# Performance work log

Measured on AMD Instinct MI355X. Metric: run time of the kernel, lower is better.

## Reference

```python
import jax, jax.numpy as jnp
import numpy as np

N_NODES = 50000
N_EDGES = 600000
D = 128
NEG_SLOPE = 0.2


def _gat_conv(x, src, dst, W, a_src, a_dst, b):
    # x: [N, D]; src/dst: [E'] (self-loops included); PyG GATConv, heads=1
    h = x @ W                               # [N, D]
    alpha_s = h @ a_src                     # [N]
    alpha_d = h @ a_dst                     # [N]
    e = alpha_s[src] + alpha_d[dst]         # [E'] raw scores per edge j->i
    e = jnp.where(e > 0, e, NEG_SLOPE * e)  # LeakyReLU(0.2)
    # segment softmax over incoming edges of each dst node
    m = jax.ops.segment_max(e, dst, num_segments=N_NODES)
    ex = jnp.exp(e - m[dst])
    denom = jax.ops.segment_sum(ex, dst, num_segments=N_NODES)
    alpha = ex / denom[dst]                 # [E']
    out = jax.ops.segment_sum(alpha[:, None] * h[src], dst, num_segments=N_NODES)
    return out + b


def setup_inputs() -> dict:
    key = jax.random.key(0)
    ks = jax.random.split(key, 10)
    scale = 1.0 / np.sqrt(D)
    x = jax.random.normal(ks[0], (N_NODES, D), dtype=jnp.float32)
    edge_index = jax.random.randint(ks[1], (2, N_EDGES), 0, N_NODES, dtype=jnp.int64)
    params = {}
    for i, base in ((1, 2), (2, 6)):
        params[f"W{i}"] = jax.random.normal(ks[base], (D, D), dtype=jnp.float32) * scale
        params[f"a_src{i}"] = jax.random.normal(ks[base + 1], (D,), dtype=jnp.float32) * scale
        params[f"a_dst{i}"] = jax.random.normal(ks[base + 2], (D,), dtype=jnp.float32) * scale
        params[f"b{i}"] = jnp.zeros((D,), dtype=jnp.float32)
    return {"x": x, "edge_index": edge_index, **params}


def reference(x, edge_index, W1, a_src1, a_dst1, b1, W2, a_src2, a_dst2, b2):
    # add self-loops (PyG GATConv default add_self_loops=True)
    loops = jnp.arange(N_NODES, dtype=edge_index.dtype)
    src = jnp.concatenate([edge_index[0], loops])
    dst = jnp.concatenate([edge_index[1], loops])
    h = _gat_conv(x, src, dst, W1, a_src1, a_dst1, b1)
    h = jax.nn.relu(h)  # BasicGNN act between layers, none after last
    out = _gat_conv(h, src, dst, W2, a_src2, a_dst2, b2)
    return out
```

## Files before the change

kernel.cpp:

```cpp
#include <hip/hip_runtime.h>
#include <hip/hip_bf16.h>

#define D 128
#define NEG_SLOPE 0.2f
#define AGG_CHUNK 128
#define CHUNKB 4096
#define CAPN 64

typedef short bf16x8 __attribute__((ext_vector_type(8)));
typedef unsigned short ushort8 __attribute__((ext_vector_type(8)));
typedef float f32x4 __attribute__((ext_vector_type(4)));

__device__ inline unsigned short bfbits(float f) {
  __hip_bfloat16 b = __float2bfloat16(f);
  return *(unsigned short*)&b;
}

__device__ inline float2 bf2_to_f2(unsigned v) {
  return make_float2(__uint_as_float(v << 16), __uint_as_float(v & 0xffff0000u));
}


template <bool RELU, bool BF16IN>
__device__ __forceinline__ void gemm_body(ushort* Wt, int tile,
                                          const void* __restrict__ in,
                                          const float* __restrict__ W,
                                          const float* __restrict__ a_s,
                                          const float* __restrict__ a_d,
                                          ushort* __restrict__ hb,
                                          float* __restrict__ as_out,
                                          float* __restrict__ ad_out, int N) {
  int tid = threadIdx.x;
  for (int u = tid; u < 2048; u += 256) {
    int kp = u >> 5, cg = u & 31;
    int k = kp * 2;
    float4 w0 = *(const float4*)(W + (size_t)k * D + cg * 4);
    float4 w1 = *(const float4*)(W + (size_t)(k + 1) * D + cg * 4);
    float v0[4] = {w0.x, w0.y, w0.z, w0.w};
    float v1[4] = {w1.x, w1.y, w1.z, w1.w};
    #pragma unroll
    for (int i = 0; i < 4; ++i) {
      int c = cg * 4 + i;
      unsigned word = (unsigned)bfbits(v0[i]) | ((unsigned)bfbits(v1[i]) << 16);
      int byte = c * 256 + ((k * 2) ^ ((c & 7) << 4));
      *(unsigned*)((char*)Wt + byte) = word;
    }
  }
  __syncthreads();

  int wave = tid >> 6, lane = tid & 63;
  int lrow = lane & 15, lgrp = lane >> 4;
  int r0 = tile * 128 + wave * 32;
  int rowA[2];
  rowA[0] = min(r0 + lrow, N - 1);
  rowA[1] = min(r0 + 16 + lrow, N - 1);

  f32x4 acc[2][8];
  #pragma unroll
  for (int t = 0; t < 2; ++t)
    #pragma unroll
    for (int nt = 0; nt < 8; ++nt) acc[t][nt] = (f32x4){0.f, 0.f, 0.f, 0.f};

  #pragma unroll
  for (int ks = 0; ks < 4; ++ks) {
    bf16x8 af[2];
    #pragma unroll
    for (int t = 0; t < 2; ++t) {
      if (BF16IN) {
        const ushort* arow = (const ushort*)in + (size_t)rowA[t] * D;
        ushort8 u = *(const ushort8*)(arow + ks * 32 + lgrp * 8);
        if (RELU) {
          #pragma unroll
          for (int j = 0; j < 8; ++j) u[j] = (u[j] & 0x8000u) ? 0 : u[j];
        }
        #pragma unroll
        for (int j = 0; j < 8; ++j) af[t][j] = (short)u[j];
      } else {
        const float* arow = (const float*)in + (size_t)rowA[t] * D;
        float4 a0 = *(const float4*)(arow + ks * 32 + lgrp * 8);
        float4 a1 = *(const float4*)(arow + ks * 32 + lgrp * 8 + 4);
        if (RELU) {
          a0.x = fmaxf(a0.x, 0.f); a0.y = fmaxf(a0.y, 0.f);
          a0.z = fmaxf(a0.z, 0.f); a0.w = fmaxf(a0.w, 0.f);
          a1.x = fmaxf(a1.x, 0.f); a1.y = fmaxf(a1.y, 0.f);
          a1.z = fmaxf(a1.z, 0.f); a1.w = fmaxf(a1.w, 0.f);
        }
        af[t][0] = (short)bfbits(a0.x); af[t][1] = (short)bfbits(a0.y);
        af[t][2] = (short)bfbits(a0.z); af[t][3] = (short)bfbits(a0.w);
        af[t][4] = (short)bfbits(a1.x); af[t][5] = (short)bfbits(a1.y);
        af[t][6] = (short)bfbits(a1.z); af[t][7] = (short)bfbits(a1.w);
      }
    }
    #pragma unroll
    for (int nt = 0; nt < 8; ++nt) {
      int c = nt * 16 + lrow;
      int kb = (ks * 64 + lgrp * 16) ^ ((c & 7) << 4);
      bf16x8 bfr = *(const bf16x8*)((const char*)Wt + c * 256 + kb);
      acc[0][nt] = __builtin_amdgcn_mfma_f32_16x16x32_bf16(af[0], bfr, acc[0][nt], 0, 0, 0);
      acc[1][nt] = __builtin_amdgcn_mfma_f32_16x16x32_bf16(af[1], bfr, acc[1][nt], 0, 0, 0);
    }
  }

  float ps[2][4] = {{0.f,0.f,0.f,0.f},{0.f,0.f,0.f,0.f}};
  float pd[2][4] = {{0.f,0.f,0.f,0.f},{0.f,0.f,0.f,0.f}};
  #pragma unroll
  for (int nt = 0; nt < 8; ++nt) {
    float asc = a_s[nt * 16 + lrow];
    float adc = a_d[nt * 16 + lrow];
    #pragma unroll
    for (int t = 0; t < 2; ++t) {
      #pragma unroll
      for (int r = 0; r < 4; ++r) {
        float v = acc[t][nt][r];
        ps[t][r] += v * asc;
        pd[t][r] += v * adc;
        int row = r0 + t * 16 + lgrp * 4 + r;
        if (row < N) hb[(size_t)row * D + nt * 16 + lrow] = bfbits(v);
      }
    }
  }
  #pragma unroll
  for (int mk = 1; mk < 16; mk <<= 1) {
    #pragma unroll
    for (int t = 0; t < 2; ++t)
      #pragma unroll
      for (int r = 0; r < 4; ++r) {
        ps[t][r] += __shfl_xor(ps[t][r], mk);
        pd[t][r] += __shfl_xor(pd[t][r], mk);
      }
  }
  if (lrow == 0) {
    #pragma unroll
    for (int t = 0; t < 2; ++t)
      #pragma unroll
      for (int r = 0; r < 4; ++r) {
        int row = r0 + t * 16 + lgrp * 4 + r;
        if (row < N) { as_out[row] = ps[t][r]; ad_out[row] = pd[t][r]; }
      }
  }
}


__global__ __launch_bounds__(256) void scatter_gemm_kernel(const int* __restrict__ ei,
                                                           int* __restrict__ cursor,
                                                           ushort* __restrict__ stage16,
                                                           int E, int total, int nblk,
                                                           const float* __restrict__ in,
                                                           const float* __restrict__ W,
                                                           const float* __restrict__ a_s,
                                                           const float* __restrict__ a_d,
                                                           ushort* __restrict__ hb,
                                                           float* __restrict__ as_out,
                                                           float* __restrict__ ad_out, int N) {
  if ((int)blockIdx.x < nblk) {
    int base = blockIdx.x * CHUNKB;
    int end = min(base + CHUNKB, total);
    for (int e = base + threadIdx.x; e < end; e += 256) {
      int src, dst;
      if (e < E) { src = ei[e]; dst = ei[E + e]; }
      else       { src = dst = e - E; }
      int pos = atomicAdd(&cursor[dst], 1);
      if (pos < CAPN) stage16[(size_t)dst * CAPN + pos] = (ushort)src;
    }
  } else {
    __shared__ ushort Wt[D * D];
    gemm_body<false, false>(Wt, blockIdx.x - nblk, in, W, a_s, a_d, hb, as_out, ad_out, N);
  }
}


__global__ __launch_bounds__(256) void gemm_bf16_kernel(const ushort* __restrict__ in,
                                                        const float* __restrict__ W,
                                                        const float* __restrict__ a_s,
                                                        const float* __restrict__ a_d,
                                                        ushort* __restrict__ hb,
                                                        float* __restrict__ as_out,
                                                        float* __restrict__ ad_out, int N) {
  __shared__ ushort Wt[D * D];
  gemm_body<true, true>(Wt, blockIdx.x, in, W, a_s, a_d, hb, as_out, ad_out, N);
}


template <typename TOUT>
__global__ __launch_bounds__(256) void agg_kernel(const ushort* __restrict__ hb,
                                                  const int* __restrict__ cursor,
                                                  const ushort* __restrict__ stage16,
                                                  const float* __restrict__ as_,
                                                  const float* __restrict__ ad_,
                                                  const float* __restrict__ bias,
                                                  TOUT* __restrict__ out, int N) {
  int wid = threadIdx.x >> 6;
  int lane = threadIdx.x & 63;
  int n = blockIdx.x * 4 + wid;
  if (n >= N) return;
  int deg = cursor[n];
  if (deg > CAPN) deg = CAPN;
  int start = n * CAPN;
  float adv = ad_[n];
  int g = lane >> 4;
  int fl = lane & 15;

  float accf[8] = {0.f, 0.f, 0.f, 0.f, 0.f, 0.f, 0.f, 0.f};
  float denom;

  if (deg <= 32) {
    int s0 = 0;
    float asv = 0.f;
    if (lane < deg) {
      s0 = (int)stage16[start + lane];
      asv = as_[s0];
    }
    uint4 pv[8];
    #pragma unroll
    for (int it = 0; it < 8; ++it) {
      int idx = it * 4 + g;
      int sv = __shfl(s0, idx < 64 ? idx : 0);
      if (idx < deg)
        pv[it] = *(const uint4*)(hb + (size_t)sv * D + fl * 8);
    }
    float w0 = 0.f;
    if (lane < deg) {
      float sc = asv + adv;
      sc = sc > 0.f ? sc : NEG_SLOPE * sc;
      w0 = __expf(sc);
    }
    denom = w0;
    #pragma unroll
    for (int off = 32; off; off >>= 1) denom += __shfl_xor(denom, off);
    #pragma unroll
    for (int it = 0; it < 8; ++it) {
      int idx = it * 4 + g;
      float wv = __shfl(w0, idx < 64 ? idx : 0);
      if (idx < deg) {
        float2 f0 = bf2_to_f2(pv[it].x), f1 = bf2_to_f2(pv[it].y);
        float2 f2 = bf2_to_f2(pv[it].z), f3 = bf2_to_f2(pv[it].w);
        accf[0] += wv * f0.x; accf[1] += wv * f0.y;
        accf[2] += wv * f1.x; accf[3] += wv * f1.y;
        accf[4] += wv * f2.x; accf[5] += wv * f2.y;
        accf[6] += wv * f3.x; accf[7] += wv * f3.y;
      }
    }
  } else {
    int end = start + deg;
    int e0 = start + lane;
    int s0 = 0;
    float w0 = 0.f;
    if (e0 < end) {
      s0 = (int)stage16[e0];
      float sc = as_[s0] + adv;
      sc = sc > 0.f ? sc : NEG_SLOPE * sc;
      w0 = __expf(sc);
    }
    denom = w0;
    #pragma unroll
    for (int off = 32; off; off >>= 1) denom += __shfl_xor(denom, off);
    for (int i = 0; i < deg; i += 4) {
      int idx = i + g;
      int   sv = __shfl(s0, idx < 64 ? idx : 0);
      float wv = __shfl(w0, idx < 64 ? idx : 0);
      if (idx < deg) {
        uint4 hv = *(const uint4*)(hb + (size_t)sv * D + fl * 8);
        float2 f0 = bf2_to_f2(hv.x), f1 = bf2_to_f2(hv.y);
        float2 f2 = bf2_to_f2(hv.z), f3 = bf2_to_f2(hv.w);
        accf[0] += wv * f0.x; accf[1] += wv * f0.y;
        accf[2] += wv * f1.x; accf[3] += wv * f1.y;
        accf[4] += wv * f2.x; accf[5] += wv * f2.y;
        accf[6] += wv * f3.x; accf[7] += wv * f3.y;
      }
    }
  }

  #pragma unroll
  for (int j = 0; j < 8; ++j) accf[j] += __shfl_xor(accf[j], 16);
  #pragma unroll
  for (int j = 0; j < 8; ++j) accf[j] += __shfl_xor(accf[j], 32);

  if (g == 0) {
    float inv = 1.f / denom;
    float4 b0 = *(const float4*)(bias + fl * 8);
    float4 b1 = *(const float4*)(bias + fl * 8 + 4);
    float o[8] = {accf[0] * inv + b0.x, accf[1] * inv + b0.y,
                  accf[2] * inv + b0.z, accf[3] * inv + b0.w,
                  accf[4] * inv + b1.x, accf[5] * inv + b1.y,
                  accf[6] * inv + b1.z, accf[7] * inv + b1.w};
    if (sizeof(TOUT) == 4) {
      float* op = (float*)out + (size_t)n * D + fl * 8;
      *(float4*)op = make_float4(o[0], o[1], o[2], o[3]);
      *(float4*)(op + 4) = make_float4(o[4], o[5], o[6], o[7]);
    } else {
      ushort8 u;
      #pragma unroll
      for (int j = 0; j < 8; ++j) u[j] = bfbits(o[j]);
      *(ushort8*)((ushort*)out + (size_t)n * D + fl * 8) = u;
    }
  }
}


extern "C" void kernel_launch(void* const* d_in, const int* in_sizes, int n_in,
                              void* d_out, int out_size, void* d_ws, size_t ws_size,
                              hipStream_t stream) {
  const float* x   = (const float*)d_in[0];
  const int*   ei  = (const int*)d_in[1];
  const float* W1  = (const float*)d_in[2];
  const float* as1 = (const float*)d_in[3];
  const float* ad1 = (const float*)d_in[4];
  const float* b1  = (const float*)d_in[5];
  const float* W2  = (const float*)d_in[6];
  const float* as2 = (const float*)d_in[7];
  const float* ad2 = (const float*)d_in[8];
  const float* b2  = (const float*)d_in[9];

  int N = in_sizes[0] / D;
  int E = in_sizes[1] / 2;
  int total = E + N;
  int nblk = (total + CHUNKB - 1) / CHUNKB;
  int nbG = (N + 127) / 128;

  char* ws = (char*)d_ws;
  size_t off = 0;
  auto alloc = [&](size_t bytes) {
    void* p = ws + off;
    off = (off + bytes + 255) & ~(size_t)255;
    return p;
  };
  ushort*   hb      = (ushort*)alloc((size_t)N * D * sizeof(ushort));
  ushort*   tmpb    = (ushort*)alloc((size_t)N * D * sizeof(ushort));
  float*    alpha_s = (float*)alloc((size_t)N * sizeof(float));
  float*    alpha_d = (float*)alloc((size_t)N * sizeof(float));
  int*      cursor  = (int*)alloc((size_t)N * sizeof(int));
  ushort*   stage16 = (ushort*)alloc((size_t)N * CAPN * sizeof(ushort));

  hipMemsetAsync(cursor, 0, (size_t)N * sizeof(int), stream);
  scatter_gemm_kernel<<<nblk + nbG, 256, 0, stream>>>(ei, cursor, stage16, E, total, nblk,
                                                      x, W1, as1, ad1, hb, alpha_s, alpha_d, N);

  agg_kernel<ushort><<<(N + 3) / 4, 256, 0, stream>>>(hb, cursor, stage16, alpha_s, alpha_d,
                                                      b1, tmpb, N);

  gemm_bf16_kernel<<<nbG, 256, 0, stream>>>(tmpb, W2, as2, ad2, hb, alpha_s, alpha_d, N);

  agg_kernel<float><<<(N + 3) / 4, 256, 0, stream>>>(hb, cursor, stage16, alpha_s, alpha_d,
                                                     b2, (float*)d_out, N);
}
```

Measured before the change: 109.5 us.

## Split fused scatter/GEMM kernel, batch scatter atomics, vectorize weight staging

Splits the combined scatter-plus-GEMM launch into a separate edge scatter kernel and a GEMM kernel. The scatter now gives each block 1024 edges and each thread four edges, issuing all loads, then all atomics, then all stores, so more memory operations are in flight. The weight transpose into shared memory now packs eight k values per thread and does one 16-byte LDS store instead of four 4-byte stores. The split adds a kernel launch and removes the overlap the fused launch had between scatter and GEMM blocks.

```diff
diff --git a/kernel.cpp b/kernel.cpp
--- a/kernel.cpp
+++ b/kernel.cpp
@@ -3,8 +3,7 @@
 
 #define D 128
 #define NEG_SLOPE 0.2f
-#define AGG_CHUNK 128
-#define CHUNKB 4096
+#define CHUNKS 1024
 #define CAPN 64
 
 typedef short bf16x8 __attribute__((ext_vector_type(8)));
@@ -32,19 +31,22 @@
                                           float* __restrict__ ad_out, int N) {
   int tid = threadIdx.x;
   for (int u = tid; u < 2048; u += 256) {
-    int kp = u >> 5, cg = u & 31;
-    int k = kp * 2;
-    float4 w0 = *(const float4*)(W + (size_t)k * D + cg * 4);
-    float4 w1 = *(const float4*)(W + (size_t)(k + 1) * D + cg * 4);
-    float v0[4] = {w0.x, w0.y, w0.z, w0.w};
-    float v1[4] = {w1.x, w1.y, w1.z, w1.w};
-    #pragma unroll
-    for (int i = 0; i < 4; ++i) {
-      int c = cg * 4 + i;
-      unsigned word = (unsigned)bfbits(v0[i]) | ((unsigned)bfbits(v1[i]) << 16);
-      int byte = c * 256 + ((k * 2) ^ ((c & 7) << 4));
-      *(unsigned*)((char*)Wt + byte) = word;
-    }
+    int c = u & 127;
+    int kq = u >> 7;
+    uint4 wv;
+    {
+      int k0 = kq * 8;
+      float f0 = W[(size_t)(k0 + 0) * D + c], f1 = W[(size_t)(k0 + 1) * D + c];
+      float f2 = W[(size_t)(k0 + 2) * D + c], f3 = W[(size_t)(k0 + 3) * D + c];
+      float f4 = W[(size_t)(k0 + 4) * D + c], f5 = W[(size_t)(k0 + 5) * D + c];
+      float f6 = W[(size_t)(k0 + 6) * D + c], f7 = W[(size_t)(k0 + 7) * D + c];
+      wv.x = (unsigned)bfbits(f0) | ((unsigned)bfbits(f1) << 16);
+      wv.y = (unsigned)bfbits(f2) | ((unsigned)bfbits(f3) << 16);
+      wv.z = (unsigned)bfbits(f4) | ((unsigned)bfbits(f5) << 16);
+      wv.w = (unsigned)bfbits(f6) | ((unsigned)bfbits(f7) << 16);
+    }
+    int byte = c * 256 + ((kq * 16) ^ ((c & 7) << 4));
+    *(uint4*)((char*)Wt + byte) = wv;
   }
   __syncthreads();
 
@@ -141,33 +143,43 @@
 }
 
 
-__global__ __launch_bounds__(256) void scatter_gemm_kernel(const int* __restrict__ ei,
-                                                           int* __restrict__ cursor,
-                                                           ushort* __restrict__ stage16,
-                                                           int E, int total, int nblk,
-                                                           const float* __restrict__ in,
-                                                           const float* __restrict__ W,
-                                                           const float* __restrict__ a_s,
-                                                           const float* __restrict__ a_d,
-                                                           ushort* __restrict__ hb,
-                                                           float* __restrict__ as_out,
-                                                           float* __restrict__ ad_out, int N) {
-  if ((int)blockIdx.x < nblk) {
-    int base = blockIdx.x * CHUNKB;
-    int end = min(base + CHUNKB, total);
-    for (int e = base + threadIdx.x; e < end; e += 256) {
-      int src, dst;
-      if (e < E) { src = ei[e]; dst = ei[E + e]; }
-      else       { src = dst = e - E; }
-      int pos = atomicAdd(&cursor[dst], 1);
-      if (pos < CAPN) stage16[(size_t)dst * CAPN + pos] = (ushort)src;
-    }
-  } else {
-    __shared__ ushort Wt[D * D];
-    gemm_body<false, false>(Wt, blockIdx.x - nblk, in, W, a_s, a_d, hb, as_out, ad_out, N);
-  }
-}
-
+__global__ __launch_bounds__(256) void scatter_kernel(const int* __restrict__ ei,
+                                                      int* __restrict__ cursor,
+                                                      ushort* __restrict__ stage16,
+                                                      int E, int total) {
+  int base = blockIdx.x * CHUNKS + threadIdx.x;
+  int srcv[4], dstv[4], posv[4];
+  bool act[4];
+  #pragma unroll
+  for (int j = 0; j < 4; ++j) {
+    int e = base + j * 256;
+    act[j] = (e < total);
+    srcv[j] = 0; dstv[j] = 0;
+    if (act[j]) {
+      if (e < E) { srcv[j] = ei[e]; dstv[j] = ei[E + e]; }
+      else       { srcv[j] = dstv[j] = e - E; }
+    }
+  }
+  #pragma unroll
+  for (int j = 0; j < 4; ++j)
+    if (act[j]) posv[j] = atomicAdd(&cursor[dstv[j]], 1);
+  #pragma unroll
+  for (int j = 0; j < 4; ++j)
+    if (act[j] && posv[j] < CAPN)
+      stage16[(size_t)dstv[j] * CAPN + posv[j]] = (ushort)srcv[j];
+}
+
+
+__global__ __launch_bounds__(256) void gemm_f32_kernel(const float* __restrict__ in,
+                                                       const float* __restrict__ W,
+                                                       const float* __restrict__ a_s,
+                                                       const float* __restrict__ a_d,
+                                                       ushort* __restrict__ hb,
+                                                       float* __restrict__ as_out,
+                                                       float* __restrict__ ad_out, int N) {
+  __shared__ ushort Wt[D * D];
+  gemm_body<false, false>(Wt, blockIdx.x, in, W, a_s, a_d, hb, as_out, ad_out, N);
+}
 
 __global__ __launch_bounds__(256) void gemm_bf16_kernel(const ushort* __restrict__ in,
                                                         const float* __restrict__ W,
@@ -314,7 +326,7 @@
   int N = in_sizes[0] / D;
   int E = in_sizes[1] / 2;
   int total = E + N;
-  int nblk = (total + CHUNKB - 1) / CHUNKB;
+  int nblkS = (total + CHUNKS - 1) / CHUNKS;
   int nbG = (N + 127) / 128;
 
   char* ws = (char*)d_ws;
@@ -332,8 +344,9 @@
   ushort*   stage16 = (ushort*)alloc((size_t)N * CAPN * sizeof(ushort));
 
   hipMemsetAsync(cursor, 0, (size_t)N * sizeof(int), stream);
-  scatter_gemm_kernel<<<nblk + nbG, 256, 0, stream>>>(ei, cursor, stage16, E, total, nblk,
-                                                      x, W1, as1, ad1, hb, alpha_s, alpha_d, N);
+  scatter_kernel<<<nblkS, 256, 0, stream>>>(ei, cursor, stage16, E, total);
+
+  gemm_f32_kernel<<<nbG, 256, 0, stream>>>(x, W1, as1, ad1, hb, alpha_s, alpha_d, N);
 
   agg_kernel<ushort><<<(N + 3) / 4, 256, 0, stream>>>(hb, cursor, stage16, alpha_s, alpha_d,
                                                       b1, tmpb, N);
```

After: 127.7 us. +16.6%, slower.
